# Kernel optimization log

Measured on AMD Instinct MI355X. Metric: run time of the kernel, lower is better.

The kernel has to match this reference:

```python
import jax, jax.numpy as jnp
import numpy as np

T, B, F, H, A, MH = 512, 256, 512, 128, 8, 64


def setup_inputs() -> dict:
    key = jax.random.key(0)
    ks = jax.random.split(key, 14)
    s = 0.05
    return {
        "x": jax.random.normal(ks[0], (T, B, F), dtype=jnp.float32),
        "done": (jax.random.uniform(ks[1], (T, B)) < 0.1).astype(jnp.float32),
        "h0": jnp.zeros((B, H), dtype=jnp.float32),
        "c0": jnp.zeros((B, H), dtype=jnp.float32),
        "W_ih": jax.random.normal(ks[2], (4 * H, F), dtype=jnp.float32) * s,
        "W_hh": jax.random.normal(ks[3], (4 * H, H), dtype=jnp.float32) * s,
        "b_ih": jnp.zeros((4 * H,), dtype=jnp.float32),
        "b_hh": jnp.zeros((4 * H,), dtype=jnp.float32),
        "W_p1": jax.random.normal(ks[4], (H, MH), dtype=jnp.float32) * s,
        "b_p1": jnp.zeros((MH,), dtype=jnp.float32),
        "W_p2": jax.random.normal(ks[5], (MH, A), dtype=jnp.float32) * s,
        "b_p2": jnp.zeros((A,), dtype=jnp.float32),
        "W_v1": jax.random.normal(ks[6], (H, MH), dtype=jnp.float32) * s,
        "b_v1": jnp.zeros((MH,), dtype=jnp.float32),
        "W_v2": jax.random.normal(ks[7], (MH, 1), dtype=jnp.float32) * s,
        "b_v2": jnp.zeros((1,), dtype=jnp.float32),
    }


def _masked_lstm(x, done, h0, c0, W_ih, W_hh, b_ih, b_hh):
    # Per-timestep LSTM with done-mask reset, as in MemoryAgent.remember().
    def step(carry, inp):
        h, c = carry
        xt, dt = inp  # xt: [B,F], dt: [B]
        m = (1.0 - dt)[:, None]
        h = h * m
        c = c * m
        gates = xt @ W_ih.T + b_ih + h @ W_hh.T + b_hh  # [B,4H]
        i, f, g, o = jnp.split(gates, 4, axis=-1)  # PyTorch gate order i,f,g,o
        i = jax.nn.sigmoid(i)
        f = jax.nn.sigmoid(f)
        g = jnp.tanh(g)
        o = jax.nn.sigmoid(o)
        c = f * c + i * g
        h = o * jnp.tanh(c)
        return (h, c), h

    (hT, cT), hs = jax.lax.scan(step, (h0, c0), (x, done))
    return hs.reshape(-1, h0.shape[-1]), hT, cT  # [T*B,H]


def reference(x, done, h0, c0, W_ih, W_hh, b_ih, b_hh,
              W_p1, b_p1, W_p2, b_p2, W_v1, b_v1, W_v2, b_v2):
    hseq, hT, cT = _masked_lstm(x, done, h0, c0, W_ih, W_hh, b_ih, b_hh)
    logits = jnp.tanh(hseq @ W_p1 + b_p1) @ W_p2 + b_p2  # [T*B,A]
    v = jnp.tanh(hseq @ W_v1 + b_v1) @ W_v2 + b_v2        # [T*B,1]
    out = jnp.concatenate([logits, v], axis=1)            # [T*B,A+1]
    return out, hT, cT
```

## Files before the change

kernel.cpp:

```cpp
#include <hip/hip_runtime.h>
#include <stdint.h>

#define T_  512
#define B_  256
#define F_  512
#define H_  128
#define MH_ 64
#define A_  8
#define OUT0 1179648
#define OUT1 32768

typedef float f32x4 __attribute__((ext_vector_type(4)));
typedef __bf16 bfrag8 __attribute__((ext_vector_type(8)));
typedef unsigned short u16;
typedef unsigned int u32;

#define WS_GATES 0u
#define WS_HSEQ  134217728u
#define WS_WIH   167772160u
#define WS_WHH   168296448u
#define WS_WP1   168427520u
#define WS_WV1   168443904u

__device__ inline u16 f2bf(float f) {
  union { float f; u32 u; } v; v.f = f;
  u32 u = v.u;
  u32 r = (u + 0x7FFFu + ((u >> 16) & 1u)) >> 16;
  return (u16)r;
}
__device__ inline float bf2f(u16 b) {
  union { u32 u; float f; } v; v.u = ((u32)b) << 16;
  return v.f;
}

__device__ inline float fexp2(float x) {
#if __has_builtin(__builtin_amdgcn_exp2f)
  return __builtin_amdgcn_exp2f(x);
#else
  return exp2f(x);
#endif
}
__device__ inline float frcp(float x) {
#if __has_builtin(__builtin_amdgcn_rcpf)
  return __builtin_amdgcn_rcpf(x);
#else
  return 1.0f / x;
#endif
}
__device__ inline float sig_(float x) {
  return frcp(1.0f + fexp2(-1.44269504f * x));
}
__device__ inline float tanh_(float x) {
  x = fminf(30.0f, fmaxf(-30.0f, x));
  float t = fexp2(2.88539008f * x);
  return (t - 1.0f) * frcp(t + 1.0f);
}
__device__ inline float sel4(f32x4 a, int q) {
  float s01 = (q & 1) ? a[1] : a[0];
  float s23 = (q & 1) ? a[3] : a[2];
  return (q & 2) ? s23 : s01;
}

__device__ inline f32x4 mfma16(bfrag8 a, bfrag8 b, f32x4 c) {
  return __builtin_amdgcn_mfma_f32_16x16x32_bf16(a, b, c, 0, 0, 0);
}

__device__ inline void gld16(const void* g, void* l) {
  __builtin_amdgcn_global_load_lds((const __attribute__((address_space(1))) void*)g,
                                   (__attribute__((address_space(3))) void*)l, 16, 0, 0);
}

__global__ __launch_bounds__(256) void k0_prep(const float* __restrict__ W_ih,
                                               const float* __restrict__ W_hh,
                                               const float* __restrict__ W_p1,
                                               const float* __restrict__ W_v1,
                                               u16* __restrict__ wih_swz,
                                               u16* __restrict__ whh_bf,
                                               u16* __restrict__ wp1s,
                                               u16* __restrict__ wv1s) {
  int idx = blockIdx.x * 256 + threadIdx.x;
  if (idx < 262144) {
    int i = idx & 7, L = (idx >> 3) & 63, kb = (idx >> 9) & 15, nt = idx >> 13;
    wih_swz[idx] = f2bf(W_ih[(nt * 16 + (L & 15)) * 512 + kb * 32 + ((L >> 4) << 3) + i]);
  } else if (idx < 262144 + 65536) {
    int j = idx - 262144;
    whh_bf[j] = f2bf(W_hh[j]);
  } else if (idx < 262144 + 65536 + 8192) {
    int j = idx - (262144 + 65536);
    int i = j & 7, L = (j >> 3) & 63, kb = (j >> 9) & 3, nt = j >> 11;
    wp1s[j] = f2bf(W_p1[(kb * 32 + ((L >> 4) << 3) + i) * 64 + nt * 16 + (L & 15)]);
  } else if (idx < 262144 + 65536 + 16384) {
    int j = idx - (262144 + 65536 + 8192);
    int i = j & 7, L = (j >> 3) & 63, kb = (j >> 9) & 3, nt = j >> 11;
    wv1s[j] = f2bf(W_v1[(kb * 32 + ((L >> 4) << 3) + i) * 64 + nt * 16 + (L & 15)]);
  }
}

__global__ __launch_bounds__(512) void k1_gates(const float* __restrict__ x,
                                                const u16* __restrict__ wih_swz,
                                                const float* __restrict__ b_ih,
                                                const float* __restrict__ b_hh,
                                                u16* __restrict__ gates) {
  __shared__ __align__(16) u16 Abuf[16 * 64 * 8];
  __shared__ __align__(16) u16 Bbuf[64 * 64 * 8];
  const int tid = threadIdx.x;
  const int lane = tid & 63;
  const int w = tid >> 6;
  const int lrow = lane >> 4, lcol = lane & 15;
  const int m0 = blockIdx.x * 128;
  const int mt0 = (w & 1) * 4, nt0 = (w >> 1) * 8;
  f32x4 acc[4][8] = {};

  for (int k0 = 0; k0 < 512; k0 += 64) {
#pragma unroll
    for (int cc = 0; cc < 8; ++cc) {
      int c = w * 8 + cc;
      int ntg = c >> 1;
      int kbg = (k0 >> 5) + (c & 1);
      gld16(wih_swz + (ntg * 16 + kbg) * 512 + lane * 8, &Bbuf[c * 512]);
    }
#pragma unroll
    for (int j = 0; j < 4; ++j) {
      int s = tid + 512 * j;
      int c = s >> 7, L = (s >> 1) & 63, hh = s & 1;
      int mt = c >> 1, kb = c & 1;
      const float4 v = *(const float4*)&x[(m0 + mt * 16 + (L & 15)) * 512 +
                                          k0 + kb * 32 + ((L >> 4) << 3) + hh * 4];
      ushort4 pk;
      pk.x = f2bf(v.x); pk.y = f2bf(v.y); pk.z = f2bf(v.z); pk.w = f2bf(v.w);
      *(ushort4*)&Abuf[(c * 64 + L) * 8 + hh * 4] = pk;
    }
    __syncthreads();
#pragma unroll
    for (int kk = 0; kk < 2; ++kk) {
      bfrag8 af[4], bfr[8];
#pragma unroll
      for (int im = 0; im < 4; ++im)
        af[im] = *(const bfrag8*)&Abuf[(((mt0 + im) * 2 + kk) * 64 + lane) * 8];
#pragma unroll
      for (int in = 0; in < 8; ++in)
        bfr[in] = *(const bfrag8*)&Bbuf[(((nt0 + in) * 2 + kk) * 64 + lane) * 8];
#pragma unroll
      for (int im = 0; im < 4; ++im)
#pragma unroll
        for (int in = 0; in < 8; ++in)
          acc[im][in] = mfma16(af[im], bfr[in], acc[im][in]);
    }
    __syncthreads();
  }
#pragma unroll
  for (int in = 0; in < 8; ++in) {
    int n = (nt0 + in) * 16 + lcol;
    float bias = b_ih[n] + b_hh[n];
#pragma unroll
    for (int im = 0; im < 4; ++im) {
      int mbase = m0 + (mt0 + im) * 16 + lrow * 4;
#pragma unroll
      for (int r = 0; r < 4; ++r)
        gates[(mbase + r) * 512 + n] = f2bf(acc[im][in][r] + bias);
    }
  }
}

__global__ __launch_bounds__(512) void k2_lstm(const float* __restrict__ done,
                                               const float* __restrict__ h0,
                                               const float* __restrict__ c0,
                                               const u16* __restrict__ whh_bf,
                                               const u16* __restrict__ gates,
                                               u16* __restrict__ hseq,
                                               float* __restrict__ dout) {
  __shared__ __align__(16) u16 h_lds[2][4][136];
  const int tid = threadIdx.x;
  const int lane = tid & 63;
  const int w = tid >> 6;
  const int lrow = lane >> 4, lcol = lane & 15;
  const int bbase = blockIdx.x * 4;
  const int jb = w * 16;
  const int q = lcol >> 2;
  const int bt = lcol & 3;
  const int hc = jb + lrow * 4 + q;
  const int brow = bbase + bt;

  bfrag8 wf[4][4];
#pragma unroll
  for (int g = 0; g < 4; ++g)
#pragma unroll
    for (int kk = 0; kk < 4; ++kk)
      wf[g][kk] = *(const bfrag8*)&whh_bf[(g * 128 + jb + lcol) * 128 + kk * 32 + lrow * 8];

  const float m0v = 1.0f - done[brow];
  h_lds[0][bt][hc] = f2bf(h0[brow * 128 + hc] * m0v);
  float c = c0[brow * 128 + hc] * m0v;
  float hfin = 0.0f;

  u32 gp[4], gpn[4];
#pragma unroll
  for (int g = 0; g < 4; ++g)
    gp[g] = gates[brow * 512 + g * 128 + hc];
  float dnx = done[B_ + brow];
  float dn2;

  for (int t = 0; t < T_; ++t) {
    const int cur = t & 1, nxt = cur ^ 1;
    __syncthreads();

    const int tn = (t + 1 < T_) ? t + 1 : T_ - 1;
    const int t2 = (t + 2 < T_) ? t + 2 : T_ - 1;
#pragma unroll
    for (int g = 0; g < 4; ++g)
      gpn[g] = gates[(tn * B_ + brow) * 512 + g * 128 + hc];
    dn2 = done[t2 * B_ + brow];
    const float live = (t < T_ - 1) ? 1.0f : 0.0f;
    const float mk = 1.0f - live * dnx;

    bfrag8 hf[4];
#pragma unroll
    for (int kk = 0; kk < 4; ++kk)
      hf[kk] = *(const bfrag8*)&h_lds[cur][bt][kk * 32 + lrow * 8];

    f32x4 acc[4] = {};
#pragma unroll
    for (int kk = 0; kk < 4; ++kk)
#pragma unroll
      for (int g = 0; g < 4; ++g)
        acc[g] = mfma16(wf[g][kk], hf[kk], acc[g]);

    float pi = sel4(acc[0], q) + bf2f((u16)gp[0]);
    float pf = sel4(acc[1], q) + bf2f((u16)gp[1]);
    float pg = sel4(acc[2], q) + bf2f((u16)gp[2]);
    float po = sel4(acc[3], q) + bf2f((u16)gp[3]);
    float iv = sig_(pi), fv = sig_(pf), gv = tanh_(pg), ov = sig_(po);
    float cc = fv * c + iv * gv;
    float hh = ov * tanh_(cc);
    c = cc * mk;
    hfin = hh;
    hseq[((t * B_ + brow) << 7) + hc] = f2bf(hh);
    h_lds[nxt][bt][hc] = f2bf(hh * mk);

#pragma unroll
    for (int g = 0; g < 4; ++g) gp[g] = gpn[g];
    dnx = dn2;
  }
  dout[OUT0 + brow * 128 + hc] = hfin;
  dout[OUT0 + OUT1 + brow * 128 + hc] = c;
}

__global__ __launch_bounds__(256) void k3_heads(const u16* __restrict__ hseq,
                                                const u16* __restrict__ wp1s,
                                                const u16* __restrict__ wv1s,
                                                const float* __restrict__ b_p1,
                                                const float* __restrict__ W_p2,
                                                const float* __restrict__ b_p2,
                                                const float* __restrict__ b_v1,
                                                const float* __restrict__ W_v2,
                                                const float* __restrict__ b_v2,
                                                float* __restrict__ out) {
  __shared__ float midp[4][16][68];
  __shared__ float midv[4][16][68];
  __shared__ float wsm[585];
  const int tid = threadIdx.x;
  const int lane = tid & 63, w = tid >> 6;
  const int lrow = lane >> 4, lcol = lane & 15;
  const int r0 = blockIdx.x * 64;

  for (int e = tid; e < 585; e += 256) {
    float v;
    if (e < 512) v = W_p2[e];
    else if (e < 576) v = W_v2[e - 512];
    else if (e < 584) v = b_p2[e - 576];
    else v = b_v2[0];
    wsm[e] = v;
  }

  const int rowA = r0 + w * 16 + lcol;
  bfrag8 af[4];
#pragma unroll
  for (int kk = 0; kk < 4; ++kk)
    af[kk] = *(const bfrag8*)&hseq[rowA * 128 + kk * 32 + lrow * 8];

#pragma unroll
  for (int nt = 0; nt < 4; ++nt) {
    f32x4 ap = {}, av = {};
#pragma unroll
    for (int kk = 0; kk < 4; ++kk) {
      ap = mfma16(af[kk], *(const bfrag8*)&wp1s[((nt * 4 + kk) * 64 + lane) * 8], ap);
      av = mfma16(af[kk], *(const bfrag8*)&wv1s[((nt * 4 + kk) * 64 + lane) * 8], av);
    }
    float bp = b_p1[nt * 16 + lcol], bv = b_v1[nt * 16 + lcol];
#pragma unroll
    for (int r = 0; r < 4; ++r) {
      midp[w][lrow * 4 + r][nt * 16 + lcol] = tanh_(ap[r] + bp);
      midv[w][lrow * 4 + r][nt * 16 + lcol] = tanh_(av[r] + bv);
    }
  }
  __syncthreads();

  for (int o = tid; o < 576; o += 256) {
    int row = o / 9;
    int a = o - row * 9;
    float s;
    if (a < 8) {
      s = wsm[576 + a];
      const float* mrow = &midp[row >> 4][row & 15][0];
#pragma unroll
      for (int n = 0; n < 64; ++n) s += mrow[n] * wsm[n * 8 + a];
    } else {
      s = wsm[584];
      const float* mrow = &midv[row >> 4][row & 15][0];
#pragma unroll
      for (int n = 0; n < 64; ++n) s += mrow[n] * wsm[512 + n];
    }
    out[(r0 + row) * 9 + a] = s;
  }
}

extern "C" void kernel_launch(void* const* d_in, const int* in_sizes, int n_in,
                              void* d_out, int out_size, void* d_ws, size_t ws_size,
                              hipStream_t stream) {
  const float* x    = (const float*)d_in[0];
  const float* done = (const float*)d_in[1];
  const float* h0   = (const float*)d_in[2];
  const float* c0   = (const float*)d_in[3];
  const float* W_ih = (const float*)d_in[4];
  const float* W_hh = (const float*)d_in[5];
  const float* b_ih = (const float*)d_in[6];
  const float* b_hh = (const float*)d_in[7];
  const float* W_p1 = (const float*)d_in[8];
  const float* b_p1 = (const float*)d_in[9];
  const float* W_p2 = (const float*)d_in[10];
  const float* b_p2 = (const float*)d_in[11];
  const float* W_v1 = (const float*)d_in[12];
  const float* b_v1 = (const float*)d_in[13];
  const float* W_v2 = (const float*)d_in[14];
  const float* b_v2 = (const float*)d_in[15];

  char* ws = (char*)d_ws;
  u16* gates   = (u16*)(ws + WS_GATES);
  u16* hseq    = (u16*)(ws + WS_HSEQ);
  u16* wih_swz = (u16*)(ws + WS_WIH);
  u16* whh_bf  = (u16*)(ws + WS_WHH);
  u16* wp1s    = (u16*)(ws + WS_WP1);
  u16* wv1s    = (u16*)(ws + WS_WV1);
  float* out = (float*)d_out;

  k0_prep<<<dim3(1344), dim3(256), 0, stream>>>(W_ih, W_hh, W_p1, W_v1,
                                                wih_swz, whh_bf, wp1s, wv1s);
  k1_gates<<<dim3(1024), dim3(512), 0, stream>>>(x, wih_swz, b_ih, b_hh, gates);
  k2_lstm<<<dim3(64), dim3(512), 0, stream>>>(done, h0, c0, whh_bf, gates, hseq, out);
  k3_heads<<<dim3(2048), dim3(256), 0, stream>>>(hseq, wp1s, wv1s, b_p1, W_p2, b_p2,
                                                 b_v1, W_v2, b_v2, out);
}
```

Before: 837.7 us.

## Stream gate GEMM operands from global and deepen LSTM gate prefetch pipeline

The input-gate GEMM drops its LDS staging and barriers. Each wave loads its x and W_ih fragments straight from global memory into registers, and the kernel asks for two blocks per CU. The recurrent LSTM kernel is unrolled by four timesteps with a four-deep register prefetch of gates and done flags. It swaps __syncthreads for a raw waitcnt+barrier and replaces the done-mask multiply with a select. Hardware bf16 conversion and a cheaper tanh form are also added, which removes the clamp and may change rounding or overflow behaviour at the extremes.

```diff
diff --git a/kernel.cpp b/kernel.cpp
--- a/kernel.cpp
+++ b/kernel.cpp
@@ -23,10 +23,9 @@
 #define WS_WV1   168443904u
 
 __device__ inline u16 f2bf(float f) {
-  union { float f; u32 u; } v; v.f = f;
-  u32 u = v.u;
-  u32 r = (u + 0x7FFFu + ((u >> 16) & 1u)) >> 16;
-  return (u16)r;
+  __bf16 b = (__bf16)f;
+  union { __bf16 b; u16 u; } v; v.b = b;
+  return v.u;
 }
 __device__ inline float bf2f(u16 b) {
   union { u32 u; float f; } v; v.u = ((u32)b) << 16;
@@ -51,9 +50,8 @@
   return frcp(1.0f + fexp2(-1.44269504f * x));
 }
 __device__ inline float tanh_(float x) {
-  x = fminf(30.0f, fmaxf(-30.0f, x));
   float t = fexp2(2.88539008f * x);
-  return (t - 1.0f) * frcp(t + 1.0f);
+  return 1.0f - 2.0f * frcp(t + 1.0f);
 }
 __device__ inline float sel4(f32x4 a, int q) {
   float s01 = (q & 1) ? a[1] : a[0];
@@ -65,9 +63,15 @@
   return __builtin_amdgcn_mfma_f32_16x16x32_bf16(a, b, c, 0, 0, 0);
 }
 
-__device__ inline void gld16(const void* g, void* l) {
-  __builtin_amdgcn_global_load_lds((const __attribute__((address_space(1))) void*)g,
-                                   (__attribute__((address_space(3))) void*)l, 16, 0, 0);
+__device__ inline void lds_barrier() {
+  __asm__ __volatile__("s_waitcnt lgkmcnt(0)\n\ts_barrier" ::: "memory");
+}
+
+__device__ inline bfrag8 cvt8(float4 a, float4 b) {
+  bfrag8 r;
+  r[0] = (__bf16)a.x; r[1] = (__bf16)a.y; r[2] = (__bf16)a.z; r[3] = (__bf16)a.w;
+  r[4] = (__bf16)b.x; r[5] = (__bf16)b.y; r[6] = (__bf16)b.z; r[7] = (__bf16)b.w;
+  return r;
 }
 
 __global__ __launch_bounds__(256) void k0_prep(const float* __restrict__ W_ih,
@@ -96,13 +100,11 @@
   }
 }
 
-__global__ __launch_bounds__(512) void k1_gates(const float* __restrict__ x,
-                                                const u16* __restrict__ wih_swz,
-                                                const float* __restrict__ b_ih,
-                                                const float* __restrict__ b_hh,
-                                                u16* __restrict__ gates) {
-  __shared__ __align__(16) u16 Abuf[16 * 64 * 8];
-  __shared__ __align__(16) u16 Bbuf[64 * 64 * 8];
+__global__ __launch_bounds__(512, 2) void k1_gates(const float* __restrict__ x,
+                                                   const u16* __restrict__ wih_swz,
+                                                   const float* __restrict__ b_ih,
+                                                   const float* __restrict__ b_hh,
+                                                   u16* __restrict__ gates) {
   const int tid = threadIdx.x;
   const int lane = tid & 63;
   const int w = tid >> 6;
@@ -111,42 +113,37 @@
   const int mt0 = (w & 1) * 4, nt0 = (w >> 1) * 8;
   f32x4 acc[4][8] = {};
 
-  for (int k0 = 0; k0 < 512; k0 += 64) {
-#pragma unroll
-    for (int cc = 0; cc < 8; ++cc) {
-      int c = w * 8 + cc;
-      int ntg = c >> 1;
-      int kbg = (k0 >> 5) + (c & 1);
-      gld16(wih_swz + (ntg * 16 + kbg) * 512 + lane * 8, &Bbuf[c * 512]);
-    }
-#pragma unroll
-    for (int j = 0; j < 4; ++j) {
-      int s = tid + 512 * j;
-      int c = s >> 7, L = (s >> 1) & 63, hh = s & 1;
-      int mt = c >> 1, kb = c & 1;
-      const float4 v = *(const float4*)&x[(m0 + mt * 16 + (L & 15)) * 512 +
-                                          k0 + kb * 32 + ((L >> 4) << 3) + hh * 4];
-      ushort4 pk;
-      pk.x = f2bf(v.x); pk.y = f2bf(v.y); pk.z = f2bf(v.z); pk.w = f2bf(v.w);
-      *(ushort4*)&Abuf[(c * 64 + L) * 8 + hh * 4] = pk;
-    }
-    __syncthreads();
+  const float* xim[4];
+#pragma unroll
+  for (int im = 0; im < 4; ++im)
+    xim[im] = x + (m0 + (mt0 + im) * 16 + lcol) * 512 + lrow * 8;
+  const u16* wbin[8];
+#pragma unroll
+  for (int in = 0; in < 8; ++in)
+    wbin[in] = wih_swz + (nt0 + in) * 8192 + lane * 8;
+
+  for (int kit = 0; kit < 8; ++kit) {
 #pragma unroll
     for (int kk = 0; kk < 2; ++kk) {
-      bfrag8 af[4], bfr[8];
+      const int cofs = kit * 64 + kk * 32;
+      const int wofs = (kit * 2 + kk) * 512;
+      bfrag8 bf[8];
+#pragma unroll
+      for (int in = 0; in < 8; ++in)
+        bf[in] = *(const bfrag8*)(wbin[in] + wofs);
+      bfrag8 af[4];
+#pragma unroll
+      for (int im = 0; im < 4; ++im) {
+        float4 v0 = *(const float4*)(xim[im] + cofs);
+        float4 v1 = *(const float4*)(xim[im] + cofs + 4);
+        af[im] = cvt8(v0, v1);
+      }
 #pragma unroll
       for (int im = 0; im < 4; ++im)
-        af[im] = *(const bfrag8*)&Abuf[(((mt0 + im) * 2 + kk) * 64 + lane) * 8];
-#pragma unroll
-      for (int in = 0; in < 8; ++in)
-        bfr[in] = *(const bfrag8*)&Bbuf[(((nt0 + in) * 2 + kk) * 64 + lane) * 8];
-#pragma unroll
-      for (int im = 0; im < 4; ++im)
 #pragma unroll
         for (int in = 0; in < 8; ++in)
-          acc[im][in] = mfma16(af[im], bfr[in], acc[im][in]);
-    }
-    __syncthreads();
+          acc[im][in] = mfma16(af[im], bf[in], acc[im][in]);
+    }
   }
 #pragma unroll
   for (int in = 0; in < 8; ++in) {
@@ -169,7 +166,7 @@
                                                const u16* __restrict__ gates,
                                                u16* __restrict__ hseq,
                                                float* __restrict__ dout) {
-  __shared__ __align__(16) u16 h_lds[2][4][136];
+  __shared__ __align__(16) u16 hbuf[2048];
   const int tid = threadIdx.x;
   const int lane = tid & 63;
   const int w = tid >> 6;
@@ -181,6 +178,11 @@
   const int hc = jb + lrow * 4 + q;
   const int brow = bbase + bt;
 
+  const int goff = brow * 512 + hc;
+  const int soff = brow * 128 + hc;
+  const int rdc = bt * 144 + lrow * 8;
+  const int wrc = bt * 144 + hc;
+
   bfrag8 wf[4][4];
 #pragma unroll
   for (int g = 0; g < 4; ++g)
@@ -189,60 +191,67 @@
       wf[g][kk] = *(const bfrag8*)&whh_bf[(g * 128 + jb + lcol) * 128 + kk * 32 + lrow * 8];
 
   const float m0v = 1.0f - done[brow];
-  h_lds[0][bt][hc] = f2bf(h0[brow * 128 + hc] * m0v);
+  hbuf[wrc] = f2bf(h0[brow * 128 + hc] * m0v);
   float c = c0[brow * 128 + hc] * m0v;
-  float hfin = 0.0f;
-
-  u32 gp[4], gpn[4];
-#pragma unroll
-  for (int g = 0; g < 4; ++g)
-    gp[g] = gates[brow * 512 + g * 128 + hc];
-  float dnx = done[B_ + brow];
-  float dn2;
-
-  for (int t = 0; t < T_; ++t) {
-    const int cur = t & 1, nxt = cur ^ 1;
-    __syncthreads();
-
-    const int tn = (t + 1 < T_) ? t + 1 : T_ - 1;
-    const int t2 = (t + 2 < T_) ? t + 2 : T_ - 1;
-#pragma unroll
-    for (int g = 0; g < 4; ++g)
-      gpn[g] = gates[(tn * B_ + brow) * 512 + g * 128 + hc];
-    dn2 = done[t2 * B_ + brow];
-    const float live = (t < T_ - 1) ? 1.0f : 0.0f;
-    const float mk = 1.0f - live * dnx;
-
-    bfrag8 hf[4];
-#pragma unroll
-    for (int kk = 0; kk < 4; ++kk)
-      hf[kk] = *(const bfrag8*)&h_lds[cur][bt][kk * 32 + lrow * 8];
-
-    f32x4 acc[4] = {};
-#pragma unroll
-    for (int kk = 0; kk < 4; ++kk)
-#pragma unroll
-      for (int g = 0; g < 4; ++g)
-        acc[g] = mfma16(wf[g][kk], hf[kk], acc[g]);
-
-    float pi = sel4(acc[0], q) + bf2f((u16)gp[0]);
-    float pf = sel4(acc[1], q) + bf2f((u16)gp[1]);
-    float pg = sel4(acc[2], q) + bf2f((u16)gp[2]);
-    float po = sel4(acc[3], q) + bf2f((u16)gp[3]);
-    float iv = sig_(pi), fv = sig_(pf), gv = tanh_(pg), ov = sig_(po);
-    float cc = fv * c + iv * gv;
-    float hh = ov * tanh_(cc);
-    c = cc * mk;
-    hfin = hh;
-    hseq[((t * B_ + brow) << 7) + hc] = f2bf(hh);
-    h_lds[nxt][bt][hc] = f2bf(hh * mk);
-
-#pragma unroll
-    for (int g = 0; g < 4; ++g) gp[g] = gpn[g];
-    dnx = dn2;
-  }
-  dout[OUT0 + brow * 128 + hc] = hfin;
-  dout[OUT0 + OUT1 + brow * 128 + hc] = c;
+  float hh = 0.0f;
+
+  u32 gp0[4], gp1[4], gp2[4], gp3[4];
+#pragma unroll
+  for (int g = 0; g < 4; ++g) {
+    gp0[g] = gates[goff + g * 128];
+    gp1[g] = gates[131072 + goff + g * 128];
+    gp2[g] = gates[262144 + goff + g * 128];
+    gp3[g] = gates[393216 + goff + g * 128];
+  }
+  float dn0 = done[256 + brow];
+  float dn1 = done[512 + brow];
+  float dn2 = done[768 + brow];
+  float dn3 = done[1024 + brow];
+
+#define K2_STEP(GP, DN, RB, WB, T, GUARD) do {                                  \
+    lds_barrier();                                                              \
+    const u16* hp = hbuf + rdc + (RB)*1024;                                     \
+    bfrag8 hf0 = *(const bfrag8*)(hp);                                          \
+    bfrag8 hf1 = *(const bfrag8*)(hp + 32);                                     \
+    bfrag8 hf2 = *(const bfrag8*)(hp + 64);                                     \
+    bfrag8 hf3 = *(const bfrag8*)(hp + 96);                                     \
+    f32x4 a0 = {}, a1 = {}, a2 = {}, a3 = {};                                   \
+    a0 = mfma16(wf[0][0], hf0, a0); a1 = mfma16(wf[1][0], hf0, a1);             \
+    a2 = mfma16(wf[2][0], hf0, a2); a3 = mfma16(wf[3][0], hf0, a3);             \
+    a0 = mfma16(wf[0][1], hf1, a0); a1 = mfma16(wf[1][1], hf1, a1);             \
+    a2 = mfma16(wf[2][1], hf1, a2); a3 = mfma16(wf[3][1], hf1, a3);             \
+    a0 = mfma16(wf[0][2], hf2, a0); a1 = mfma16(wf[1][2], hf2, a1);             \
+    a2 = mfma16(wf[2][2], hf2, a2); a3 = mfma16(wf[3][2], hf2, a3);             \
+    a0 = mfma16(wf[0][3], hf3, a0); a1 = mfma16(wf[1][3], hf3, a1);             \
+    a2 = mfma16(wf[2][3], hf3, a2); a3 = mfma16(wf[3][3], hf3, a3);             \
+    float pi = sel4(a0, q) + bf2f((u16)GP[0]);                                  \
+    float pf = sel4(a1, q) + bf2f((u16)GP[1]);                                  \
+    float pg = sel4(a2, q) + bf2f((u16)GP[2]);                                  \
+    float po = sel4(a3, q) + bf2f((u16)GP[3]);                                  \
+    { int tg = (T) + 4; if (tg > 511) tg = 511;                                 \
+      const u16* gb = gates + (size_t)tg * 131072 + goff;                       \
+      GP[0] = gb[0]; GP[1] = gb[128]; GP[2] = gb[256]; GP[3] = gb[384]; }       \
+    bool rs = (DN != 0.0f) && (GUARD);                                          \
+    { int td = (T) + 5; if (td > 511) td = 511; DN = done[td * 256 + brow]; }   \
+    float iv = sig_(pi), fv = sig_(pf), gv = tanh_(pg), ov = sig_(po);          \
+    float cc = fv * c + iv * gv;                                                \
+    hh = ov * tanh_(cc);                                                        \
+    c = rs ? 0.0f : cc;                                                         \
+    u16 hb = f2bf(hh);                                                          \
+    hseq[(size_t)(T) * 32768 + soff] = hb;                                      \
+    hbuf[wrc + (WB)*1024] = rs ? (u16)0 : hb;                                   \
+  } while (0)
+
+  for (int tt = 0; tt < T_; tt += 4) {
+    K2_STEP(gp0, dn0, 0, 1, tt,     true);
+    K2_STEP(gp1, dn1, 1, 0, tt + 1, true);
+    K2_STEP(gp2, dn2, 0, 1, tt + 2, true);
+    K2_STEP(gp3, dn3, 1, 0, tt + 3, (tt < 508));
+  }
+#undef K2_STEP
+
+  dout[OUT0 + soff] = hh;
+  dout[OUT0 + OUT1 + soff] = c;
 }
 
 __global__ __launch_bounds__(256) void k3_heads(const u16* __restrict__ hseq,
```

New measurement: 864.4 us. 1.03x slower.
